# Kernel tuning notes

Measured on AMD Instinct MI355X. Metric: run time of the kernel, lower is better.

## Reference

```python
import jax, jax.numpy as jnp
import numpy as np

B, T, D, H = 2, 2048, 1024, 16
HD = D // H

def setup_inputs() -> dict:
    key = jax.random.key(0)
    ks = jax.random.split(key, 5)
    fan = D
    bound_w = float(np.sqrt(6.0 / fan))  # kaiming_uniform-ish scale
    return {
        "x": jax.random.normal(ks[0], (B, T, D), dtype=jnp.float32),
        "W_qkv": jax.random.uniform(ks[1], (3 * D, D), minval=-bound_w, maxval=bound_w, dtype=jnp.float32),
        "b_qkv": jax.random.uniform(ks[2], (3 * D,), minval=-bound_w, maxval=bound_w, dtype=jnp.float32),
        "W_proj": jax.random.uniform(ks[3], (D, D), minval=-bound_w, maxval=bound_w, dtype=jnp.float32),
        "b_proj": jax.random.uniform(ks[4], (D,), minval=-bound_w, maxval=bound_w, dtype=jnp.float32),
    }

def reference(x, W_qkv, b_qkv, W_proj, b_proj):
    Bx, Tx, C = x.shape
    h, hd = H, C // H
    qkv = x @ W_qkv.T + b_qkv                      # (B,T,3C)
    q, k, v = jnp.split(qkv, 3, axis=-1)
    # (B,T,C) -> (B,h,T,hd)
    q = q.reshape(Bx, Tx, h, hd).transpose(0, 2, 1, 3)
    k = k.reshape(Bx, Tx, h, hd).transpose(0, 2, 1, 3)
    v = v.reshape(Bx, Tx, h, hd).transpose(0, 2, 1, 3)
    scale = hd ** -0.5
    scores = jnp.einsum('bhqd,bhkd->bhqk', q, k) * scale
    causal = jnp.tril(jnp.ones((Tx, Tx), dtype=bool))
    scores = jnp.where(causal, scores, -jnp.inf)
    weights = jax.nn.softmax(scores, axis=-1)      # stable softmax, same math
    out = jnp.einsum('bhqk,bhkd->bhqd', weights, v)
    out = out.transpose(0, 2, 1, 3).reshape(Bx, Tx, C)
    return out @ W_proj.T + b_proj
```

## Files before the change

### kernel.cpp

```cpp
#include <hip/hip_runtime.h>

typedef unsigned short u16;
typedef __attribute__((ext_vector_type(8))) short bf16x8;
typedef __attribute__((ext_vector_type(4))) float f32x4;

#define Bb 2
#define Tt 2048
#define Dd 1024
#define Hh 16
#define HD 64
#define NTOK (Bb*Tt)
#define QKVN (3*Dd)

__device__ __forceinline__ u16 f2b(float f) {
    unsigned u = __float_as_uint(f);
    unsigned r = (u + 0x7fffu + ((u >> 16) & 1u)) >> 16;
    return (u16)r;
}

__device__ __forceinline__ void g2l16(const u16* g, u16* l) {
    __builtin_amdgcn_global_load_lds(
        (const __attribute__((address_space(1))) unsigned int*)g,
        (__attribute__((address_space(3))) unsigned int*)l,
        16, 0, 0);
}

__device__ __forceinline__ unsigned pk2(float lo, float hi) {
    return __builtin_amdgcn_perm(__float_as_uint(hi), __float_as_uint(lo), 0x07060302u);
}

#define N4X  (NTOK * Dd / 4)
#define N4WQ (3 * Dd * Dd / 4)
#define N4WP (Dd * Dd / 4)
__global__ void cvt_all(const float* __restrict__ x, const float* __restrict__ wq,
                        const float* __restrict__ wp, u16* __restrict__ xb,
                        u16* __restrict__ wqb, u16* __restrict__ wpb) {
    int i = blockIdx.x * blockDim.x + threadIdx.x;
    const float* src; u16* dst; int j;
    if (i < N4X)                { src = x;  dst = xb;  j = i; }
    else if (i < N4X + N4WQ)    { src = wq; dst = wqb; j = i - N4X; }
    else                        { src = wp; dst = wpb; j = i - N4X - N4WQ; }
    float4 f = ((const float4*)src)[j];
    ushort4 o;
    o.x = f2b(f.x); o.y = f2b(f.y); o.z = f2b(f.z); o.w = f2b(f.w);
    ((ushort4*)dst)[j] = o;
}

#define TRS 136

__global__ __launch_bounds__(256, 3)
void gemm_qkv(const u16* __restrict__ A, const u16* __restrict__ Bt,
              const float* __restrict__ bias,
              u16* __restrict__ C16, u16* __restrict__ Vt) {
    const int N = QKVN, K = Dd;
    __shared__ alignas(16) u16 smem[128 * TRS];
    u16* As = smem;
    u16* Bs = smem + 8192;
    const int tid = threadIdx.x;
    const int wave = tid >> 6, lane = tid & 63;
    const int quad = lane >> 4, l16 = lane & 15;
    const int wm = (wave & 1) * 64, wn = (wave >> 1) * 64;
    const int m0 = blockIdx.x * 128, n0 = blockIdx.y * 128;
    const int lrow = lane >> 2, lcol = (lane & 3) << 3;

    f32x4 acc[4][4];
#pragma unroll
    for (int i = 0; i < 4; ++i)
#pragma unroll
        for (int j = 0; j < 4; ++j)
            acc[i][j] = (f32x4){0.f, 0.f, 0.f, 0.f};

    for (int k0 = 0; k0 < K; k0 += 64) {
#pragma unroll
        for (int h = 0; h < 2; ++h)
#pragma unroll
            for (int c = 0; c < 2; ++c) {
                const int rb = (c * 4 + wave) * 16;
                g2l16(A  + (size_t)(m0 + rb + lrow) * K + k0 + h * 32 + lcol,
                      &As[h * 4096 + rb * 32 + (lane << 3)]);
                g2l16(Bt + (size_t)(n0 + rb + lrow) * K + k0 + h * 32 + lcol,
                      &Bs[h * 4096 + rb * 32 + (lane << 3)]);
            }
        __syncthreads();
        bf16x8 a[4][2], b[4][2];
#pragma unroll
        for (int h = 0; h < 2; ++h) {
#pragma unroll
            for (int i = 0; i < 4; ++i)
                a[i][h] = *(const bf16x8*)(&As[h * 4096 + (wm + i * 16 + l16) * 32 + quad * 8]);
#pragma unroll
            for (int i = 0; i < 4; ++i)
                b[i][h] = *(const bf16x8*)(&Bs[h * 4096 + (wn + i * 16 + l16) * 32 + quad * 8]);
        }
#pragma unroll
        for (int h = 0; h < 2; ++h)
#pragma unroll
            for (int i = 0; i < 4; ++i)
#pragma unroll
                for (int j = 0; j < 4; ++j)
                    acc[i][j] = __builtin_amdgcn_mfma_f32_16x16x32_bf16(a[i][h], b[j][h], acc[i][j], 0, 0, 0);
        __syncthreads();
    }

    float b4[4];
#pragma unroll
    for (int j = 0; j < 4; ++j) b4[j] = bias[n0 + wn + j * 16 + l16];
    const bool isV = (n0 >= 2 * Dd);

    if (!isV) {
#pragma unroll
        for (int i = 0; i < 4; ++i)
#pragma unroll
            for (int j = 0; j < 4; ++j)
#pragma unroll
                for (int r = 0; r < 4; ++r) {
                    int m = m0 + wm + i * 16 + quad * 4 + r;
                    int n = n0 + wn + j * 16 + l16;
                    C16[(size_t)m * N + n] = f2b(acc[i][j][r] + b4[j]);
                }
    } else {
#pragma unroll
        for (int i = 0; i < 4; ++i)
#pragma unroll
            for (int j = 0; j < 4; ++j)
#pragma unroll
                for (int r = 0; r < 4; ++r) {
                    int ml = wm + i * 16 + quad * 4 + r;
                    int nl = wn + j * 16 + l16;
                    smem[nl * TRS + ml] = f2b(acc[i][j][r] + b4[j]);
                }
        __syncthreads();
        const int bidx = m0 >> 11, t0 = m0 & 2047;
        const int nl = tid >> 1, toff = (tid & 1) * 64;
        u16* dst = Vt + (size_t)bidx * (Hh * HD * Tt)
                      + (size_t)(n0 - 2 * Dd + nl) * Tt + t0 + toff;
        const u16* srcl = &smem[nl * TRS + toff];
#pragma unroll
        for (int k = 0; k < 8; ++k)
            *(uint4*)(dst + k * 8) = *(const uint4*)(srcl + k * 8);
    }
}

__global__ __launch_bounds__(256, 2)
void gemm_proj(const u16* __restrict__ A, const u16* __restrict__ Bt,
               const float* __restrict__ bias, float* __restrict__ Co) {
    const int N = Dd, K = Dd;
    __shared__ alignas(16) u16 As[2 * 128 * 32];
    __shared__ alignas(16) u16 Bs[2 * 64 * 32];
    const int tid = threadIdx.x;
    const int wave = tid >> 6, lane = tid & 63;
    const int quad = lane >> 4, l16 = lane & 15;
    const int wm = (wave & 1) * 64, wn = (wave >> 1) * 32;
    const int m0 = blockIdx.x * 128, n0 = blockIdx.y * 64;
    const int lrow = lane >> 2, lcol = (lane & 3) << 3;

    f32x4 acc[4][2];
#pragma unroll
    for (int i = 0; i < 4; ++i)
#pragma unroll
        for (int j = 0; j < 2; ++j)
            acc[i][j] = (f32x4){0.f, 0.f, 0.f, 0.f};

    for (int k0 = 0; k0 < K; k0 += 64) {
#pragma unroll
        for (int h = 0; h < 2; ++h) {
#pragma unroll
            for (int c = 0; c < 2; ++c) {
                const int rb = (c * 4 + wave) * 16;
                g2l16(A + (size_t)(m0 + rb + lrow) * K + k0 + h * 32 + lcol,
                      &As[h * 4096 + rb * 32 + (lane << 3)]);
            }
            g2l16(Bt + (size_t)(n0 + wave * 16 + lrow) * K + k0 + h * 32 + lcol,
                  &Bs[h * 2048 + (wave * 16) * 32 + (lane << 3)]);
        }
        __syncthreads();
        bf16x8 a[4][2], b[2][2];
#pragma unroll
        for (int h = 0; h < 2; ++h) {
#pragma unroll
            for (int i = 0; i < 4; ++i)
                a[i][h] = *(const bf16x8*)(&As[h * 4096 + (wm + i * 16 + l16) * 32 + quad * 8]);
#pragma unroll
            for (int j = 0; j < 2; ++j)
                b[j][h] = *(const bf16x8*)(&Bs[h * 2048 + (wn + j * 16 + l16) * 32 + quad * 8]);
        }
#pragma unroll
        for (int h = 0; h < 2; ++h)
#pragma unroll
            for (int i = 0; i < 4; ++i)
#pragma unroll
                for (int j = 0; j < 2; ++j)
                    acc[i][j] = __builtin_amdgcn_mfma_f32_16x16x32_bf16(a[i][h], b[j][h], acc[i][j], 0, 0, 0);
        __syncthreads();
    }

    float b2[2];
#pragma unroll
    for (int j = 0; j < 2; ++j) b2[j] = bias[n0 + wn + j * 16 + l16];

#pragma unroll
    for (int i = 0; i < 4; ++i)
#pragma unroll
        for (int j = 0; j < 2; ++j)
#pragma unroll
            for (int r = 0; r < 4; ++r) {
                int m = m0 + wm + i * 16 + quad * 4 + r;
                int n = n0 + wn + j * 16 + l16;
                Co[(size_t)m * N + n] = acc[i][j][r] + b2[j];
            }
}

#define LKP 80
#define PSP 84
#define FMX 24.0f

__global__ __launch_bounds__(256, 3)
void attn_fwd(const u16* __restrict__ qkv, const u16* __restrict__ Vt,
              u16* __restrict__ Ao) {
    const int pair = blockIdx.x, bh = blockIdx.y;
    const int hh = bh & (Hh - 1), bidx = bh >> 4;
    const u16* Qp = qkv + (size_t)bidx * Tt * QKVN + hh * HD;
    const u16* Kp = Qp + Dd;
    const u16* Vp = Vt + (size_t)bh * HD * Tt;
    const int tid = threadIdx.x;
    const int wave = tid >> 6, lane = tid & 63;
    const int quad = lane >> 4, l16 = lane & 15;

    __shared__ alignas(16) u16 Ks[2][64 * LKP];
    __shared__ alignas(16) u16 Vs[2][64 * LKP];
    __shared__ alignas(16) u16 Ps[4][16 * PSP];
    u16* Pw = &Ps[wave][0];

    const int srow = tid >> 3, scol = (tid & 7) << 3;
    const int st0 = srow * LKP + scol, st1 = (srow + 32) * LKP + scol;
    const float sc = 0.125f * 1.44269504f;

    float mb[16];
#pragma unroll
    for (int nt = 0; nt < 4; ++nt)
#pragma unroll
        for (int r = 0; r < 4; ++r)
            mb[nt * 4 + r] = (nt * 16 + quad * 4 + r <= wave * 16 + l16) ? -FMX : -250.0f;

    for (int half = 0; half < 2; ++half) {
        const int qt = half ? pair : (31 - pair);
        const int qrow_g = qt * 64 + wave * 16 + l16;
        bf16x8 aq[2];
#pragma unroll
        for (int kk = 0; kk < 2; ++kk)
            aq[kk] = *(const bf16x8*)(Qp + (size_t)qrow_g * QKVN + kk * 32 + quad * 8);

        f32x4 o[4];
#pragma unroll
        for (int nt = 0; nt < 4; ++nt) o[nt] = (f32x4){0.f, 0.f, 0.f, 0.f};
        float lsum = 0.f;

        {
            uint4 k0r = *(const uint4*)(Kp + (size_t)srow * QKVN + scol);
            uint4 k1r = *(const uint4*)(Kp + (size_t)(srow + 32) * QKVN + scol);
            uint4 v0r = *(const uint4*)(Vp + (size_t)srow * Tt + scol);
            uint4 v1r = *(const uint4*)(Vp + (size_t)(srow + 32) * Tt + scol);
            *(uint4*)(&Ks[0][st0]) = k0r;
            *(uint4*)(&Ks[0][st1]) = k1r;
            *(uint4*)(&Vs[0][st0]) = v0r;
            *(uint4*)(&Vs[0][st1]) = v1r;
        }
        __syncthreads();

        const u16* kp0 = Kp + (size_t)(64 + srow) * QKVN + scol;
        const u16* kp1 = kp0 + (size_t)32 * QKVN;
        const u16* vp0 = Vp + (size_t)srow * Tt + 64 + scol;
        const u16* vp1 = vp0 + (size_t)32 * Tt;

        u16* Kcur = &Ks[0][0]; u16* Knxt = &Ks[1][0];
        u16* Vcur = &Vs[0][0]; u16* Vnxt = &Vs[1][0];

        for (int kt = 0; kt < qt; ++kt) {
            uint4 k0r = *(const uint4*)kp0;
            uint4 k1r = *(const uint4*)kp1;
            uint4 v0r = *(const uint4*)vp0;
            uint4 v1r = *(const uint4*)vp1;
            kp0 += (size_t)64 * QKVN; kp1 += (size_t)64 * QKVN;
            vp0 += 64; vp1 += 64;

            f32x4 s[4];
#pragma unroll
            for (int nt = 0; nt < 4; ++nt) {
                f32x4 z = (f32x4){0.f, 0.f, 0.f, 0.f};
#pragma unroll
                for (int kk = 0; kk < 2; ++kk) {
                    bf16x8 ak = *(const bf16x8*)(&Kcur[(nt * 16 + l16) * LKP + kk * 32 + quad * 8]);
                    z = __builtin_amdgcn_mfma_f32_16x16x32_bf16(ak, aq[kk], z, 0, 0, 0);
                }
                s[nt] = z;
            }

#pragma unroll
            for (int nt = 0; nt < 4; ++nt)
#pragma unroll
                for (int r = 0; r < 4; ++r) {
                    float p = exp2f(__builtin_fmaf(s[nt][r], sc, -FMX));
                    s[nt][r] = p;
                    lsum += p;
                }

#pragma unroll
            for (int nt = 0; nt < 4; ++nt) {
                uint2 d;
                d.x = pk2(s[nt][0], s[nt][1]);
                d.y = pk2(s[nt][2], s[nt][3]);
                *(uint2*)(&Pw[l16 * PSP + nt * 16 + quad * 4]) = d;
            }

#pragma unroll
            for (int kk = 0; kk < 2; ++kk) {
                bf16x8 bp = *(const bf16x8*)(&Pw[l16 * PSP + kk * 32 + quad * 8]);
#pragma unroll
                for (int nt = 0; nt < 4; ++nt) {
                    bf16x8 av = *(const bf16x8*)(&Vcur[(nt * 16 + l16) * LKP + kk * 32 + quad * 8]);
                    o[nt] = __builtin_amdgcn_mfma_f32_16x16x32_bf16(av, bp, o[nt], 0, 0, 0);
                }
            }

            *(uint4*)(&Knxt[st0]) = k0r;
            *(uint4*)(&Knxt[st1]) = k1r;
            *(uint4*)(&Vnxt[st0]) = v0r;
            *(uint4*)(&Vnxt[st1]) = v1r;
            u16* t;
            t = Kcur; Kcur = Knxt; Knxt = t;
            t = Vcur; Vcur = Vnxt; Vnxt = t;
            __syncthreads();
        }

        {
            f32x4 s[4];
#pragma unroll
            for (int nt = 0; nt < 4; ++nt) {
                f32x4 z = (f32x4){0.f, 0.f, 0.f, 0.f};
#pragma unroll
                for (int kk = 0; kk < 2; ++kk) {
                    bf16x8 ak = *(const bf16x8*)(&Kcur[(nt * 16 + l16) * LKP + kk * 32 + quad * 8]);
                    z = __builtin_amdgcn_mfma_f32_16x16x32_bf16(ak, aq[kk], z, 0, 0, 0);
                }
                s[nt] = z;
            }
#pragma unroll
            for (int nt = 0; nt < 4; ++nt)
#pragma unroll
                for (int r = 0; r < 4; ++r) {
                    float p = exp2f(__builtin_fmaf(s[nt][r], sc, mb[nt * 4 + r]));
                    s[nt][r] = p;
                    lsum += p;
                }
#pragma unroll
            for (int nt = 0; nt < 4; ++nt) {
                uint2 d;
                d.x = pk2(s[nt][0], s[nt][1]);
                d.y = pk2(s[nt][2], s[nt][3]);
                *(uint2*)(&Pw[l16 * PSP + nt * 16 + quad * 4]) = d;
            }
#pragma unroll
            for (int kk = 0; kk < 2; ++kk) {
                bf16x8 bp = *(const bf16x8*)(&Pw[l16 * PSP + kk * 32 + quad * 8]);
#pragma unroll
                for (int nt = 0; nt < 4; ++nt) {
                    bf16x8 av = *(const bf16x8*)(&Vcur[(nt * 16 + l16) * LKP + kk * 32 + quad * 8]);
                    o[nt] = __builtin_amdgcn_mfma_f32_16x16x32_bf16(av, bp, o[nt], 0, 0, 0);
                }
            }
        }
        __syncthreads();

        lsum += __shfl_xor(lsum, 16, 64);
        lsum += __shfl_xor(lsum, 32, 64);
        const float rinv = 1.0f / lsum;
        u16* orow = Ao + ((size_t)bidx * Tt + qrow_g) * Dd + hh * HD;
#pragma unroll
        for (int nt = 0; nt < 4; ++nt) {
            ushort4 p4;
            p4.x = f2b(o[nt][0] * rinv); p4.y = f2b(o[nt][1] * rinv);
            p4.z = f2b(o[nt][2] * rinv); p4.w = f2b(o[nt][3] * rinv);
            *(ushort4*)(orow + nt * 16 + quad * 4) = p4;
        }
    }
}

extern "C" void kernel_launch(void* const* d_in, const int* in_sizes, int n_in,
                              void* d_out, int out_size, void* d_ws, size_t ws_size,
                              hipStream_t stream) {
    const float* x      = (const float*)d_in[0];
    const float* W_qkv  = (const float*)d_in[1];
    const float* b_qkv  = (const float*)d_in[2];
    const float* W_proj = (const float*)d_in[3];
    const float* b_proj = (const float*)d_in[4];
    float* out = (float*)d_out;

    char* ws = (char*)d_ws;
    u16* Wprojb = (u16*)(ws);
    u16* Wqkvb  = (u16*)(ws + (2u << 20));
    u16* xb     = (u16*)(ws + (8u << 20));
    u16* qkvb   = (u16*)(ws + (16u << 20));
    u16* Vtb    = (u16*)(ws + (40u << 20));
    u16* attnb  = (u16*)(ws + (2u << 20));

    cvt_all<<<(N4X + N4WQ + N4WP) / 256, 256, 0, stream>>>(x, W_qkv, W_proj, xb, Wqkvb, Wprojb);

    {
        dim3 grid(NTOK / 128, QKVN / 128);
        gemm_qkv<<<grid, 256, 0, stream>>>(xb, Wqkvb, b_qkv, qkvb, Vtb);
    }
    {
        dim3 grid(16, Bb * Hh);
        attn_fwd<<<grid, 256, 0, stream>>>(qkvb, Vtb, attnb);
    }
    {
        dim3 grid(NTOK / 128, Dd / 64);
        gemm_proj<<<grid, 256, 0, stream>>>(attnb, Wprojb, b_proj, out);
    }
}
```

Before: 179.1 us.

## Process both query tiles of a causal pair in one shared K/V sweep

The attention kernel no longer handles its low and high query tiles one after the other. It now streams K/V once and computes both tiles together while the low tile is still active, so each staged K/V tile serves both, then continues with the high tile alone. This removes about half of the K/V global loads and LDS staging for the overlapping range, and a blockIdx-based mirroring of the pair index is added for balance. In exchange the kernel holds twice the accumulators and Q fragments and twice the P scratch, so launch bounds drop from 3 to 2 blocks per SM, which lowers occupancy.

```diff
diff --git a/kernel.cpp b/kernel.cpp
--- a/kernel.cpp
+++ b/kernel.cpp
@@ -214,10 +214,71 @@
 #define PSP 84
 #define FMX 24.0f
 
-__global__ __launch_bounds__(256, 3)
+#define MFMA16(a,b,c) __builtin_amdgcn_mfma_f32_16x16x32_bf16(a, b, c, 0, 0, 0)
+
+template<bool LIGHT, bool MASKH, bool MASKL>
+__device__ __forceinline__ void attn_iter(
+    const u16* Kcur, const u16* Vcur, u16* PwH, u16* PwL,
+    const bf16x8 (&aqH)[2], const bf16x8 (&aqL)[2],
+    f32x4 (&oH)[4], f32x4 (&oL)[4], float& lsH, float& lsL,
+    const float (&mb)[16], int l16, int quad, float sc)
+{
+    f32x4 sH[4], sL[4];
+#pragma unroll
+    for (int nt = 0; nt < 4; ++nt) {
+        f32x4 zH = (f32x4){0.f, 0.f, 0.f, 0.f};
+        f32x4 zL = (f32x4){0.f, 0.f, 0.f, 0.f};
+#pragma unroll
+        for (int kk = 0; kk < 2; ++kk) {
+            bf16x8 ak = *(const bf16x8*)(&Kcur[(nt * 16 + l16) * LKP + kk * 32 + quad * 8]);
+            zH = MFMA16(ak, aqH[kk], zH);
+            if (LIGHT) zL = MFMA16(ak, aqL[kk], zL);
+        }
+        sH[nt] = zH;
+        if (LIGHT) sL[nt] = zL;
+    }
+#pragma unroll
+    for (int nt = 0; nt < 4; ++nt)
+#pragma unroll
+        for (int r = 0; r < 4; ++r) {
+            float pH = exp2f(__builtin_fmaf(sH[nt][r], sc, MASKH ? mb[nt * 4 + r] : -FMX));
+            sH[nt][r] = pH; lsH += pH;
+            if (LIGHT) {
+                float pL = exp2f(__builtin_fmaf(sL[nt][r], sc, MASKL ? mb[nt * 4 + r] : -FMX));
+                sL[nt][r] = pL; lsL += pL;
+            }
+        }
+#pragma unroll
+    for (int nt = 0; nt < 4; ++nt) {
+        uint2 d;
+        d.x = pk2(sH[nt][0], sH[nt][1]); d.y = pk2(sH[nt][2], sH[nt][3]);
+        *(uint2*)(&PwH[l16 * PSP + nt * 16 + quad * 4]) = d;
+        if (LIGHT) {
+            uint2 e;
+            e.x = pk2(sL[nt][0], sL[nt][1]); e.y = pk2(sL[nt][2], sL[nt][3]);
+            *(uint2*)(&PwL[l16 * PSP + nt * 16 + quad * 4]) = e;
+        }
+    }
+#pragma unroll
+    for (int kk = 0; kk < 2; ++kk) {
+        bf16x8 bpH = *(const bf16x8*)(&PwH[l16 * PSP + kk * 32 + quad * 8]);
+        bf16x8 bpL;
+        if (LIGHT) bpL = *(const bf16x8*)(&PwL[l16 * PSP + kk * 32 + quad * 8]);
+#pragma unroll
+        for (int nt = 0; nt < 4; ++nt) {
+            bf16x8 av = *(const bf16x8*)(&Vcur[(nt * 16 + l16) * LKP + kk * 32 + quad * 8]);
+            oH[nt] = MFMA16(av, bpH, oH[nt]);
+            if (LIGHT) oL[nt] = MFMA16(av, bpL, oL[nt]);
+        }
+    }
+}
+
+__global__ __launch_bounds__(256, 2)
 void attn_fwd(const u16* __restrict__ qkv, const u16* __restrict__ Vt,
               u16* __restrict__ Ao) {
-    const int pair = blockIdx.x, bh = blockIdx.y;
+    const int p = ((int)blockIdx.y < 16) ? (int)blockIdx.x : 15 - (int)blockIdx.x;
+    const int qtH = 31 - p, qtL = p;
+    const int bh = blockIdx.y;
     const int hh = bh & (Hh - 1), bidx = bh >> 4;
     const u16* Qp = qkv + (size_t)bidx * Tt * QKVN + hh * HD;
     const u16* Kp = Qp + Dd;
@@ -228,8 +289,9 @@
 
     __shared__ alignas(16) u16 Ks[2][64 * LKP];
     __shared__ alignas(16) u16 Vs[2][64 * LKP];
-    __shared__ alignas(16) u16 Ps[4][16 * PSP];
-    u16* Pw = &Ps[wave][0];
+    __shared__ alignas(16) u16 Ps[4][2][16 * PSP];
+    u16* PwH = &Ps[wave][0][0];
+    u16* PwL = &Ps[wave][1][0];
 
     const int srow = tid >> 3, scol = (tid & 7) << 3;
     const int st0 = srow * LKP + scol, st1 = (srow + 32) * LKP + scol;
@@ -242,146 +304,86 @@
         for (int r = 0; r < 4; ++r)
             mb[nt * 4 + r] = (nt * 16 + quad * 4 + r <= wave * 16 + l16) ? -FMX : -250.0f;
 
-    for (int half = 0; half < 2; ++half) {
-        const int qt = half ? pair : (31 - pair);
-        const int qrow_g = qt * 64 + wave * 16 + l16;
-        bf16x8 aq[2];
-#pragma unroll
-        for (int kk = 0; kk < 2; ++kk)
-            aq[kk] = *(const bf16x8*)(Qp + (size_t)qrow_g * QKVN + kk * 32 + quad * 8);
-
-        f32x4 o[4];
-#pragma unroll
-        for (int nt = 0; nt < 4; ++nt) o[nt] = (f32x4){0.f, 0.f, 0.f, 0.f};
-        float lsum = 0.f;
-
-        {
-            uint4 k0r = *(const uint4*)(Kp + (size_t)srow * QKVN + scol);
-            uint4 k1r = *(const uint4*)(Kp + (size_t)(srow + 32) * QKVN + scol);
-            uint4 v0r = *(const uint4*)(Vp + (size_t)srow * Tt + scol);
-            uint4 v1r = *(const uint4*)(Vp + (size_t)(srow + 32) * Tt + scol);
-            *(uint4*)(&Ks[0][st0]) = k0r;
-            *(uint4*)(&Ks[0][st1]) = k1r;
-            *(uint4*)(&Vs[0][st0]) = v0r;
-            *(uint4*)(&Vs[0][st1]) = v1r;
-        }
-        __syncthreads();
-
-        const u16* kp0 = Kp + (size_t)(64 + srow) * QKVN + scol;
-        const u16* kp1 = kp0 + (size_t)32 * QKVN;
-        const u16* vp0 = Vp + (size_t)srow * Tt + 64 + scol;
-        const u16* vp1 = vp0 + (size_t)32 * Tt;
-
-        u16* Kcur = &Ks[0][0]; u16* Knxt = &Ks[1][0];
-        u16* Vcur = &Vs[0][0]; u16* Vnxt = &Vs[1][0];
-
-        for (int kt = 0; kt < qt; ++kt) {
-            uint4 k0r = *(const uint4*)kp0;
-            uint4 k1r = *(const uint4*)kp1;
-            uint4 v0r = *(const uint4*)vp0;
-            uint4 v1r = *(const uint4*)vp1;
-            kp0 += (size_t)64 * QKVN; kp1 += (size_t)64 * QKVN;
-            vp0 += 64; vp1 += 64;
-
-            f32x4 s[4];
-#pragma unroll
-            for (int nt = 0; nt < 4; ++nt) {
-                f32x4 z = (f32x4){0.f, 0.f, 0.f, 0.f};
-#pragma unroll
-                for (int kk = 0; kk < 2; ++kk) {
-                    bf16x8 ak = *(const bf16x8*)(&Kcur[(nt * 16 + l16) * LKP + kk * 32 + quad * 8]);
-                    z = __builtin_amdgcn_mfma_f32_16x16x32_bf16(ak, aq[kk], z, 0, 0, 0);
-                }
-                s[nt] = z;
-            }
-
-#pragma unroll
-            for (int nt = 0; nt < 4; ++nt)
-#pragma unroll
-                for (int r = 0; r < 4; ++r) {
-                    float p = exp2f(__builtin_fmaf(s[nt][r], sc, -FMX));
-                    s[nt][r] = p;
-                    lsum += p;
-                }
-
-#pragma unroll
-            for (int nt = 0; nt < 4; ++nt) {
-                uint2 d;
-                d.x = pk2(s[nt][0], s[nt][1]);
-                d.y = pk2(s[nt][2], s[nt][3]);
-                *(uint2*)(&Pw[l16 * PSP + nt * 16 + quad * 4]) = d;
-            }
-
-#pragma unroll
-            for (int kk = 0; kk < 2; ++kk) {
-                bf16x8 bp = *(const bf16x8*)(&Pw[l16 * PSP + kk * 32 + quad * 8]);
-#pragma unroll
-                for (int nt = 0; nt < 4; ++nt) {
-                    bf16x8 av = *(const bf16x8*)(&Vcur[(nt * 16 + l16) * LKP + kk * 32 + quad * 8]);
-                    o[nt] = __builtin_amdgcn_mfma_f32_16x16x32_bf16(av, bp, o[nt], 0, 0, 0);
-                }
-            }
-
-            *(uint4*)(&Knxt[st0]) = k0r;
-            *(uint4*)(&Knxt[st1]) = k1r;
-            *(uint4*)(&Vnxt[st0]) = v0r;
-            *(uint4*)(&Vnxt[st1]) = v1r;
-            u16* t;
-            t = Kcur; Kcur = Knxt; Knxt = t;
-            t = Vcur; Vcur = Vnxt; Vnxt = t;
-            __syncthreads();
-        }
-
-        {
-            f32x4 s[4];
-#pragma unroll
-            for (int nt = 0; nt < 4; ++nt) {
-                f32x4 z = (f32x4){0.f, 0.f, 0.f, 0.f};
-#pragma unroll
-                for (int kk = 0; kk < 2; ++kk) {
-                    bf16x8 ak = *(const bf16x8*)(&Kcur[(nt * 16 + l16) * LKP + kk * 32 + quad * 8]);
-                    z = __builtin_amdgcn_mfma_f32_16x16x32_bf16(ak, aq[kk], z, 0, 0, 0);
-                }
-                s[nt] = z;
-            }
-#pragma unroll
-            for (int nt = 0; nt < 4; ++nt)
-#pragma unroll
-                for (int r = 0; r < 4; ++r) {
-                    float p = exp2f(__builtin_fmaf(s[nt][r], sc, mb[nt * 4 + r]));
-                    s[nt][r] = p;
-                    lsum += p;
-                }
-#pragma unroll
-            for (int nt = 0; nt < 4; ++nt) {
-                uint2 d;
-                d.x = pk2(s[nt][0], s[nt][1]);
-                d.y = pk2(s[nt][2], s[nt][3]);
-                *(uint2*)(&Pw[l16 * PSP + nt * 16 + quad * 4]) = d;
-            }
-#pragma unroll
-            for (int kk = 0; kk < 2; ++kk) {
-                bf16x8 bp = *(const bf16x8*)(&Pw[l16 * PSP + kk * 32 + quad * 8]);
-#pragma unroll
-                for (int nt = 0; nt < 4; ++nt) {
-                    bf16x8 av = *(const bf16x8*)(&Vcur[(nt * 16 + l16) * LKP + kk * 32 + quad * 8]);
-                    o[nt] = __builtin_amdgcn_mfma_f32_16x16x32_bf16(av, bp, o[nt], 0, 0, 0);
-                }
-            }
-        }
-        __syncthreads();
-
-        lsum += __shfl_xor(lsum, 16, 64);
-        lsum += __shfl_xor(lsum, 32, 64);
-        const float rinv = 1.0f / lsum;
-        u16* orow = Ao + ((size_t)bidx * Tt + qrow_g) * Dd + hh * HD;
-#pragma unroll
-        for (int nt = 0; nt < 4; ++nt) {
-            ushort4 p4;
-            p4.x = f2b(o[nt][0] * rinv); p4.y = f2b(o[nt][1] * rinv);
-            p4.z = f2b(o[nt][2] * rinv); p4.w = f2b(o[nt][3] * rinv);
-            *(ushort4*)(orow + nt * 16 + quad * 4) = p4;
-        }
+    const int qrowH = qtH * 64 + wave * 16 + l16;
+    const int qrowL = qtL * 64 + wave * 16 + l16;
+    bf16x8 aqH[2], aqL[2];
+#pragma unroll
+    for (int kk = 0; kk < 2; ++kk) {
+        aqH[kk] = *(const bf16x8*)(Qp + (size_t)qrowH * QKVN + kk * 32 + quad * 8);
+        aqL[kk] = *(const bf16x8*)(Qp + (size_t)qrowL * QKVN + kk * 32 + quad * 8);
+    }
+
+    f32x4 oH[4], oL[4];
+#pragma unroll
+    for (int nt = 0; nt < 4; ++nt) {
+        oH[nt] = (f32x4){0.f, 0.f, 0.f, 0.f};
+        oL[nt] = (f32x4){0.f, 0.f, 0.f, 0.f};
+    }
+    float lsH = 0.f, lsL = 0.f;
+
+    {
+        uint4 k0r = *(const uint4*)(Kp + (size_t)srow * QKVN + scol);
+        uint4 k1r = *(const uint4*)(Kp + (size_t)(srow + 32) * QKVN + scol);
+        uint4 v0r = *(const uint4*)(Vp + (size_t)srow * Tt + scol);
+        uint4 v1r = *(const uint4*)(Vp + (size_t)(srow + 32) * Tt + scol);
+        *(uint4*)(&Ks[0][st0]) = k0r;
+        *(uint4*)(&Ks[0][st1]) = k1r;
+        *(uint4*)(&Vs[0][st0]) = v0r;
+        *(uint4*)(&Vs[0][st1]) = v1r;
+    }
+    __syncthreads();
+
+    const u16* kp0 = Kp + (size_t)(64 + srow) * QKVN + scol;
+    const u16* kp1 = kp0 + (size_t)32 * QKVN;
+    const u16* vp0 = Vp + (size_t)srow * Tt + 64 + scol;
+    const u16* vp1 = vp0 + (size_t)32 * Tt;
+    u16* Kcur = &Ks[0][0]; u16* Knxt = &Ks[1][0];
+    u16* Vcur = &Vs[0][0]; u16* Vnxt = &Vs[1][0];
+
+#define PREFETCH \
+    uint4 k0r = *(const uint4*)kp0, k1r = *(const uint4*)kp1; \
+    uint4 v0r = *(const uint4*)vp0, v1r = *(const uint4*)vp1; \
+    kp0 += (size_t)64 * QKVN; kp1 += (size_t)64 * QKVN; vp0 += 64; vp1 += 64;
+
+#define STAGE_SWAP \
+    *(uint4*)(&Knxt[st0]) = k0r; *(uint4*)(&Knxt[st1]) = k1r; \
+    *(uint4*)(&Vnxt[st0]) = v0r; *(uint4*)(&Vnxt[st1]) = v1r; \
+    { u16* t = Kcur; Kcur = Knxt; Knxt = t; t = Vcur; Vcur = Vnxt; Vnxt = t; } \
+    __syncthreads();
+
+    for (int kt = 0; kt < qtL; ++kt) {
+        PREFETCH
+        attn_iter<true, false, false>(Kcur, Vcur, PwH, PwL, aqH, aqL, oH, oL, lsH, lsL, mb, l16, quad, sc);
+        STAGE_SWAP
+    }
+    {
+        PREFETCH
+        attn_iter<true, false, true>(Kcur, Vcur, PwH, PwL, aqH, aqL, oH, oL, lsH, lsL, mb, l16, quad, sc);
+        STAGE_SWAP
+    }
+    for (int kt = qtL + 1; kt < qtH; ++kt) {
+        PREFETCH
+        attn_iter<false, false, false>(Kcur, Vcur, PwH, PwL, aqH, aqL, oH, oL, lsH, lsL, mb, l16, quad, sc);
+        STAGE_SWAP
+    }
+    attn_iter<false, true, false>(Kcur, Vcur, PwH, PwL, aqH, aqL, oH, oL, lsH, lsL, mb, l16, quad, sc);
+
+    lsH += __shfl_xor(lsH, 16, 64);
+    lsH += __shfl_xor(lsH, 32, 64);
+    lsL += __shfl_xor(lsL, 16, 64);
+    lsL += __shfl_xor(lsL, 32, 64);
+    const float rH = 1.0f / lsH, rL = 1.0f / lsL;
+    u16* orowH = Ao + ((size_t)bidx * Tt + qrowH) * Dd + hh * HD;
+    u16* orowL = Ao + ((size_t)bidx * Tt + qrowL) * Dd + hh * HD;
+#pragma unroll
+    for (int nt = 0; nt < 4; ++nt) {
+        ushort4 pH, pL;
+        pH.x = f2b(oH[nt][0] * rH); pH.y = f2b(oH[nt][1] * rH);
+        pH.z = f2b(oH[nt][2] * rH); pH.w = f2b(oH[nt][3] * rH);
+        *(ushort4*)(orowH + nt * 16 + quad * 4) = pH;
+        pL.x = f2b(oL[nt][0] * rL); pL.y = f2b(oL[nt][1] * rL);
+        pL.z = f2b(oL[nt][2] * rL); pL.w = f2b(oL[nt][3] * rL);
+        *(ushort4*)(orowL + nt * 16 + quad * 4) = pL;
     }
 }
 
```

Measured after the change: 181.6 us. No clear change (+1.4%).

## Deepen K/V register prefetch to two tiles and use raw LDS-only barriers

Applied to the files above, without the earlier changes.

The attention inner loop now prefetches K/V tiles from global memory two iterations ahead into registers instead of one, giving each global load a full extra iteration of MFMA work to hide behind. The __syncthreads calls are replaced with an inline s_waitcnt lgkmcnt(0) plus s_barrier, which waits only on LDS traffic and not on outstanding global loads (vmcnt). This keeps the in-flight prefetches from stalling the barrier. It costs more live registers, which may lower occupancy, and correctness depends on the compiler inserting vmcnt waits before the prefetched registers are used.

```diff
diff --git a/kernel.cpp b/kernel.cpp
--- a/kernel.cpp
+++ b/kernel.cpp
@@ -28,6 +28,8 @@
 __device__ __forceinline__ unsigned pk2(float lo, float hi) {
     return __builtin_amdgcn_perm(__float_as_uint(hi), __float_as_uint(lo), 0x07060302u);
 }
+
+#define RAW_BARRIER() asm volatile("s_waitcnt lgkmcnt(0)\n\ts_barrier" ::: "memory")
 
 #define N4X  (NTOK * Dd / 4)
 #define N4WQ (3 * Dd * Dd / 4)
@@ -255,33 +257,43 @@
         for (int nt = 0; nt < 4; ++nt) o[nt] = (f32x4){0.f, 0.f, 0.f, 0.f};
         float lsum = 0.f;
 
+        const u16* kp = Kp + (size_t)srow * QKVN + scol;
+        const u16* vp = Vp + (size_t)srow * Tt + scol;
+        uint4 ck0, ck1, cv0, cv1;
         {
-            uint4 k0r = *(const uint4*)(Kp + (size_t)srow * QKVN + scol);
-            uint4 k1r = *(const uint4*)(Kp + (size_t)(srow + 32) * QKVN + scol);
-            uint4 v0r = *(const uint4*)(Vp + (size_t)srow * Tt + scol);
-            uint4 v1r = *(const uint4*)(Vp + (size_t)(srow + 32) * Tt + scol);
-            *(uint4*)(&Ks[0][st0]) = k0r;
-            *(uint4*)(&Ks[0][st1]) = k1r;
-            *(uint4*)(&Vs[0][st0]) = v0r;
-            *(uint4*)(&Vs[0][st1]) = v1r;
-        }
-        __syncthreads();
-
-        const u16* kp0 = Kp + (size_t)(64 + srow) * QKVN + scol;
-        const u16* kp1 = kp0 + (size_t)32 * QKVN;
-        const u16* vp0 = Vp + (size_t)srow * Tt + 64 + scol;
-        const u16* vp1 = vp0 + (size_t)32 * Tt;
+            uint4 t0k0 = *(const uint4*)(kp);
+            uint4 t0k1 = *(const uint4*)(kp + (size_t)32 * QKVN);
+            uint4 t0v0 = *(const uint4*)(vp);
+            uint4 t0v1 = *(const uint4*)(vp + (size_t)32 * Tt);
+            if (qt >= 1) {
+                ck0 = *(const uint4*)(kp + (size_t)64 * QKVN);
+                ck1 = *(const uint4*)(kp + (size_t)96 * QKVN);
+                cv0 = *(const uint4*)(vp + 64);
+                cv1 = *(const uint4*)(vp + (size_t)32 * Tt + 64);
+            }
+            *(uint4*)(&Ks[0][st0]) = t0k0;
+            *(uint4*)(&Ks[0][st1]) = t0k1;
+            *(uint4*)(&Vs[0][st0]) = t0v0;
+            *(uint4*)(&Vs[0][st1]) = t0v1;
+        }
+        RAW_BARRIER();
+        kp += (size_t)128 * QKVN;
+        vp += 128;
 
         u16* Kcur = &Ks[0][0]; u16* Knxt = &Ks[1][0];
         u16* Vcur = &Vs[0][0]; u16* Vnxt = &Vs[1][0];
 
         for (int kt = 0; kt < qt; ++kt) {
-            uint4 k0r = *(const uint4*)kp0;
-            uint4 k1r = *(const uint4*)kp1;
-            uint4 v0r = *(const uint4*)vp0;
-            uint4 v1r = *(const uint4*)vp1;
-            kp0 += (size_t)64 * QKVN; kp1 += (size_t)64 * QKVN;
-            vp0 += 64; vp1 += 64;
+            uint4 nk0, nk1, nv0, nv1;
+            const bool more2 = (kt + 2 <= qt);
+            if (more2) {
+                nk0 = *(const uint4*)(kp);
+                nk1 = *(const uint4*)(kp + (size_t)32 * QKVN);
+                nv0 = *(const uint4*)(vp);
+                nv1 = *(const uint4*)(vp + (size_t)32 * Tt);
+                kp += (size_t)64 * QKVN;
+                vp += 64;
+            }
 
             f32x4 s[4];
 #pragma unroll
@@ -294,7 +306,6 @@
                 }
                 s[nt] = z;
             }
-
 #pragma unroll
             for (int nt = 0; nt < 4; ++nt)
 #pragma unroll
@@ -303,7 +314,6 @@
                     s[nt][r] = p;
                     lsum += p;
                 }
-
 #pragma unroll
             for (int nt = 0; nt < 4; ++nt) {
                 uint2 d;
@@ -311,7 +321,6 @@
                 d.y = pk2(s[nt][2], s[nt][3]);
                 *(uint2*)(&Pw[l16 * PSP + nt * 16 + quad * 4]) = d;
             }
-
 #pragma unroll
             for (int kk = 0; kk < 2; ++kk) {
                 bf16x8 bp = *(const bf16x8*)(&Pw[l16 * PSP + kk * 32 + quad * 8]);
@@ -322,14 +331,15 @@
                 }
             }
 
-            *(uint4*)(&Knxt[st0]) = k0r;
-            *(uint4*)(&Knxt[st1]) = k1r;
-            *(uint4*)(&Vnxt[st0]) = v0r;
-            *(uint4*)(&Vnxt[st1]) = v1r;
+            *(uint4*)(&Knxt[st0]) = ck0;
+            *(uint4*)(&Knxt[st1]) = ck1;
+            *(uint4*)(&Vnxt[st0]) = cv0;
+            *(uint4*)(&Vnxt[st1]) = cv1;
+            RAW_BARRIER();
             u16* t;
             t = Kcur; Kcur = Knxt; Knxt = t;
             t = Vcur; Vcur = Vnxt; Vnxt = t;
-            __syncthreads();
+            if (more2) { ck0 = nk0; ck1 = nk1; cv0 = nv0; cv1 = nv1; }
         }
 
         {
@@ -369,7 +379,7 @@
                 }
             }
         }
-        __syncthreads();
+        RAW_BARRIER();
 
         lsum += __shfl_xor(lsum, 16, 64);
         lsum += __shfl_xor(lsum, 32, 64);
```

Result: slower. 189.6 us (+5.8%).
